# Kernel optimization log

Measured on AMD Instinct MI355X. Metric: run time of the kernel, lower is better.

The kernel has to match this reference:

```python
import jax, jax.numpy as jnp
import numpy as np

DIM = 1024
N = 65536

def _l2norm(x):
    # F.normalize: x / max(||x||_2, eps) along last dim, eps=1e-12
    n = jnp.linalg.norm(x, axis=-1, keepdims=True)
    return x / jnp.maximum(n, 1e-12)

def setup_inputs() -> dict:
    key = jax.random.key(0)
    ks = jax.random.split(key, 10)
    s = 0.02
    return {
        "q_init": jax.random.normal(ks[0], (1, DIM), jnp.float32),
        "k_init": jax.random.normal(ks[1], (N, DIM), jnp.float32),
        "Wq": jax.random.normal(ks[2], (DIM, DIM // 2), jnp.float32) * s,
        "bq": jnp.zeros((DIM // 2,), jnp.float32),
        "Wk": jax.random.normal(ks[3], (DIM, DIM // 2), jnp.float32) * s,
        "bk": jnp.zeros((DIM // 2,), jnp.float32),
        "Wv": jax.random.normal(ks[4], (DIM, DIM), jnp.float32) * s,
        "bv": jnp.zeros((DIM,), jnp.float32),
        "Wm": jax.random.normal(ks[5], (DIM, DIM), jnp.float32) * s,
        "bm": jnp.zeros((DIM,), jnp.float32),
        "gamma": jnp.ones((1,), jnp.float32),
    }

def reference(q_init, k_init, Wq, bq, Wk, bk, Wv, bv, Wm, bm, gamma):
    q = _l2norm(q_init) @ Wq + bq              # [1, dim/2]
    kn = _l2norm(k_init)                        # [N, dim]
    k = kn @ Wk + bk                            # [N, dim/2]
    v = kn @ Wv + bv                            # [N, dim]
    scores = q @ k.T                            # [1, N]
    # global mean/std rescale (torch.std is unbiased, ddof=1)
    scores = (scores - scores.mean()) / (jnp.std(scores, ddof=1) + 1e-8)
    attn = jax.nn.softmax(jnp.clip(scores, -10.0, 10.0), axis=-1)
    # dropout is identity in eval mode
    out = (attn @ v) @ Wm + bm                  # [1, dim]
    g = jax.nn.sigmoid(gamma)                   # [1]
    return g * q_init + (1.0 - g) * out
```

## Files before the change

### kernel.cpp

```cpp
#include <hip/hip_runtime.h>
#include <math.h>

#define DIM   1024
#define HALF  512
#define NROWS 65536
#define SBLK  4096
#define WBLK  1024
#define WF1   32

#define OFF_QN     0
#define OFF_QACC   (OFF_QN + DIM)
#define OFF_PVEC   (OFF_QACC + HALF)
#define OFF_SCAL   (OFF_PVEC + DIM)
#define OFF_PSTAT  (OFF_SCAL + 8)
#define OFF_S      (OFF_PSTAT + 2*SBLK)
#define OFF_INVN   (OFF_S + NROWS)
#define OFF_COEFF  (OFF_INVN + NROWS)
#define OFF_ESUM   (OFF_COEFF + NROWS)
#define OFF_PW     (OFF_ESUM + 256)
#define OFF_P2     (OFF_PW + WBLK*DIM)
#define OFF_WACC   (OFF_P2 + WF1*DIM)
#define OFF_OVACC  (OFF_WACC + DIM)
#define OFF_OUTACC (OFF_OVACC + DIM)
#define OFF_END    (OFF_OUTACC + DIM)

__global__ void k_qnorm(const float* __restrict__ q_init, float* __restrict__ qn) {
    __shared__ float red[1024];
    int t = threadIdx.x;
    float v = q_init[t];
    red[t] = v * v;
    __syncthreads();
    for (int s = 512; s > 0; s >>= 1) {
        if (t < s) red[t] += red[t + s];
        __syncthreads();
    }
    float inv = 1.0f / fmaxf(sqrtf(red[0]), 1e-12f);
    qn[t] = v * inv;
}

__global__ void k_matvec_col(const float* __restrict__ M,
                             const float* __restrict__ coeff,
                             const float* __restrict__ cbias,
                             float* __restrict__ out,
                             int nrows, int ncols4) {
    __shared__ float4 red[256];
    int t = threadIdx.x, c4 = blockIdx.x;
    const float4* M4 = (const float4*)M;
    float4 acc = make_float4(0.f, 0.f, 0.f, 0.f);
    for (int r = t; r < nrows; r += 256) {
        float c = coeff[r];
        if (cbias) c += cbias[r];
        float4 m = M4[(size_t)r * ncols4 + c4];
        acc.x += c * m.x; acc.y += c * m.y; acc.z += c * m.z; acc.w += c * m.w;
    }
    red[t] = acc;
    __syncthreads();
    for (int s = 128; s > 0; s >>= 1) {
        if (t < s) {
            red[t].x += red[t + s].x; red[t].y += red[t + s].y;
            red[t].z += red[t + s].z; red[t].w += red[t + s].w;
        }
        __syncthreads();
    }
    if (t == 0) ((float4*)out)[c4] = red[0];
}

__global__ void k_pvec(const float* __restrict__ Wk,
                       const float* __restrict__ qacc,
                       const float* __restrict__ bq,
                       float* __restrict__ pvec) {
    __shared__ float q[HALF];
    int t = threadIdx.x;
    for (int j = t; j < HALF; j += 256) q[j] = qacc[j] + bq[j];
    __syncthreads();
    int wave = t >> 6, lane = t & 63;
    int d = blockIdx.x * 4 + wave;
    const float* row = Wk + (size_t)d * HALF;
    float acc = 0.f;
    #pragma unroll
    for (int j0 = 0; j0 < HALF; j0 += 64) acc += row[j0 + lane] * q[j0 + lane];
    #pragma unroll
    for (int o = 32; o > 0; o >>= 1) acc += __shfl_down(acc, o);
    if (lane == 0) pvec[d] = acc;
}

__global__ void k_scores(const float* __restrict__ K,
                         const float* __restrict__ pvec,
                         float* __restrict__ svals,
                         float* __restrict__ invn,
                         float2* __restrict__ pstat) {
    __shared__ float4 p4s[256];
    __shared__ float wsum[4], wssq[4];
    int t = threadIdx.x;
    p4s[t] = ((const float4*)pvec)[t];
    __syncthreads();
    int wave = t >> 6, lane = t & 63;
    int row0 = blockIdx.x * 16 + wave * 4;
    const float4* k4 = (const float4*)K + (size_t)row0 * 256;
    float d0 = 0, d1 = 0, d2 = 0, d3 = 0;
    float q0 = 0, q1 = 0, q2 = 0, q3 = 0;
    #pragma unroll
    for (int i = 0; i < 4; ++i) {
        int idx = lane + i * 64;
        float4 p = p4s[idx];
        float4 a = k4[idx];
        float4 b = k4[256 + idx];
        float4 c = k4[512 + idx];
        float4 e = k4[768 + idx];
        d0 += a.x * p.x + a.y * p.y + a.z * p.z + a.w * p.w;
        q0 += a.x * a.x + a.y * a.y + a.z * a.z + a.w * a.w;
        d1 += b.x * p.x + b.y * p.y + b.z * p.z + b.w * p.w;
        q1 += b.x * b.x + b.y * b.y + b.z * b.z + b.w * b.w;
        d2 += c.x * p.x + c.y * p.y + c.z * p.z + c.w * p.w;
        q2 += c.x * c.x + c.y * c.y + c.z * c.z + c.w * c.w;
        d3 += e.x * p.x + e.y * p.y + e.z * p.z + e.w * p.w;
        q3 += e.x * e.x + e.y * e.y + e.z * e.z + e.w * e.w;
    }
    #pragma unroll
    for (int o = 32; o > 0; o >>= 1) {
        d0 += __shfl_down(d0, o); q0 += __shfl_down(q0, o);
        d1 += __shfl_down(d1, o); q1 += __shfl_down(q1, o);
        d2 += __shfl_down(d2, o); q2 += __shfl_down(q2, o);
        d3 += __shfl_down(d3, o); q3 += __shfl_down(q3, o);
    }
    if (lane == 0) {
        float i0 = 1.0f / fmaxf(sqrtf(q0), 1e-12f);
        float i1 = 1.0f / fmaxf(sqrtf(q1), 1e-12f);
        float i2 = 1.0f / fmaxf(sqrtf(q2), 1e-12f);
        float i3 = 1.0f / fmaxf(sqrtf(q3), 1e-12f);
        float s0 = d0 * i0, s1 = d1 * i1, s2 = d2 * i2, s3 = d3 * i3;
        float4 sv = make_float4(s0, s1, s2, s3);
        float4 iv = make_float4(i0, i1, i2, i3);
        *(float4*)(svals + row0) = sv;
        *(float4*)(invn + row0) = iv;
        wsum[wave] = s0 + s1 + s2 + s3;
        wssq[wave] = s0 * s0 + s1 * s1 + s2 * s2 + s3 * s3;
    }
    __syncthreads();
    if (t == 0)
        pstat[blockIdx.x] = make_float2(wsum[0] + wsum[1] + wsum[2] + wsum[3],
                                        wssq[0] + wssq[1] + wssq[2] + wssq[3]);
}

__global__ void k_redstats(const float2* __restrict__ pstat, float* __restrict__ scal) {
    __shared__ float rs[1024], rq[1024];
    int t = threadIdx.x;
    float s = 0.f, q = 0.f;
    for (int i = t; i < SBLK; i += 1024) {
        float2 p = pstat[i];
        s += p.x; q += p.y;
    }
    rs[t] = s; rq[t] = q;
    __syncthreads();
    for (int k = 512; k > 0; k >>= 1) {
        if (t < k) { rs[t] += rs[t + k]; rq[t] += rq[t + k]; }
        __syncthreads();
    }
    if (t == 0) {
        float mean = rs[0] / (float)NROWS;
        float var  = (rq[0] - (float)NROWS * mean * mean) / (float)(NROWS - 1);
        scal[0] = mean;
        scal[1] = 1.0f / (sqrtf(fmaxf(var, 0.0f)) + 1e-8f);
    }
}

__global__ void k_coeff(const float* __restrict__ svals,
                        const float* __restrict__ invn,
                        const float* __restrict__ scal,
                        float* __restrict__ coeff,
                        float* __restrict__ esum) {
    __shared__ float red[256];
    int t = threadIdx.x;
    int i = blockIdx.x * 256 + t;
    float mean = scal[0], rstd = scal[1];
    float z = (svals[i] - mean) * rstd;
    z = fminf(fmaxf(z, -10.0f), 10.0f);
    float e = expf(z);
    coeff[i] = e * invn[i];
    red[t] = e;
    __syncthreads();
    for (int s = 128; s > 0; s >>= 1) {
        if (t < s) red[t] += red[t + s];
        __syncthreads();
    }
    if (t == 0) esum[blockIdx.x] = red[0];
}

__global__ void k_wsum(const float* __restrict__ K,
                       const float* __restrict__ coeff,
                       float* __restrict__ pw) {
    int t = threadIdx.x;
    int r0 = blockIdx.x * 64;
    const float4* M4 = (const float4*)K + (size_t)r0 * 256 + t;
    const float* cf = coeff + r0;
    float4 acc = make_float4(0.f, 0.f, 0.f, 0.f);
    #pragma unroll 16
    for (int r = 0; r < 64; ++r) {
        float c = cf[r];
        float4 m = M4[(size_t)r * 256];
        acc.x += c * m.x; acc.y += c * m.y; acc.z += c * m.z; acc.w += c * m.w;
    }
    ((float4*)pw)[(size_t)blockIdx.x * 256 + t] = acc;
}

__global__ void k_wfold(const float* __restrict__ pw, float* __restrict__ p2) {
    int t = threadIdx.x, b = blockIdx.x;
    const float4* pw4 = (const float4*)pw;
    float4 acc = make_float4(0.f, 0.f, 0.f, 0.f);
    #pragma unroll
    for (int p = 0; p < WBLK / WF1; ++p) {
        float4 m = pw4[(size_t)(b * (WBLK / WF1) + p) * 256 + t];
        acc.x += m.x; acc.y += m.y; acc.z += m.z; acc.w += m.w;
    }
    ((float4*)p2)[b * 256 + t] = acc;
}

__global__ void k_wreduce(const float* __restrict__ p2,
                          const float* __restrict__ esum,
                          float* __restrict__ wacc) {
    __shared__ float red[256];
    int t = threadIdx.x;
    if (t < 256) red[t] = esum[t];
    __syncthreads();
    for (int s = 128; s > 0; s >>= 1) {
        if (t < s) red[t] += red[t + s];
        __syncthreads();
    }
    float inv = 1.0f / red[0];
    float acc = 0.f;
    #pragma unroll
    for (int b = 0; b < WF1; ++b) acc += p2[b * DIM + t];
    wacc[t] = acc * inv;
}

__global__ void k_final(const float* __restrict__ q_init,
                        const float* __restrict__ outacc,
                        const float* __restrict__ bm,
                        const float* __restrict__ gamma,
                        float* __restrict__ out) {
    int t = threadIdx.x;
    float g = 1.0f / (1.0f + expf(-gamma[0]));
    out[t] = g * q_init[t] + (1.0f - g) * (outacc[t] + bm[t]);
}

extern "C" void kernel_launch(void* const* d_in, const int* in_sizes, int n_in,
                              void* d_out, int out_size, void* d_ws, size_t ws_size,
                              hipStream_t stream) {
    const float* q_init = (const float*)d_in[0];
    const float* k_init = (const float*)d_in[1];
    const float* Wq     = (const float*)d_in[2];
    const float* bq     = (const float*)d_in[3];
    const float* Wk     = (const float*)d_in[4];
    const float* Wv     = (const float*)d_in[6];
    const float* bv     = (const float*)d_in[7];
    const float* Wm     = (const float*)d_in[8];
    const float* bm     = (const float*)d_in[9];
    const float* gamma  = (const float*)d_in[10];
    float* out = (float*)d_out;
    float* ws  = (float*)d_ws;

    float*  qn     = ws + OFF_QN;
    float*  qacc   = ws + OFF_QACC;
    float*  pvec   = ws + OFF_PVEC;
    float*  scal   = ws + OFF_SCAL;
    float2* pstat  = (float2*)(ws + OFF_PSTAT);
    float*  svals  = ws + OFF_S;
    float*  invn   = ws + OFF_INVN;
    float*  coeff  = ws + OFF_COEFF;
    float*  esum   = ws + OFF_ESUM;
    float*  pw     = ws + OFF_PW;
    float*  p2     = ws + OFF_P2;
    float*  wacc   = ws + OFF_WACC;
    float*  ovacc  = ws + OFF_OVACC;
    float*  outacc = ws + OFF_OUTACC;

    k_qnorm<<<1, 1024, 0, stream>>>(q_init, qn);
    k_matvec_col<<<HALF / 4, 256, 0, stream>>>(Wq, qn, nullptr, qacc, DIM, HALF / 4);
    k_pvec<<<DIM / 4, 256, 0, stream>>>(Wk, qacc, bq, pvec);
    k_scores<<<SBLK, 256, 0, stream>>>(k_init, pvec, svals, invn, pstat);
    k_redstats<<<1, 1024, 0, stream>>>(pstat, scal);
    k_coeff<<<NROWS / 256, 256, 0, stream>>>(svals, invn, scal, coeff, esum);
    k_wsum<<<WBLK, 256, 0, stream>>>(k_init, coeff, pw);
    k_wfold<<<WF1, 256, 0, stream>>>(pw, p2);
    k_wreduce<<<1, 1024, 0, stream>>>(p2, esum, wacc);
    k_matvec_col<<<DIM / 4, 256, 0, stream>>>(Wv, wacc, nullptr, ovacc, DIM, DIM / 4);
    k_matvec_col<<<DIM / 4, 256, 0, stream>>>(Wm, ovacc, bv, outacc, DIM, DIM / 4);
    k_final<<<1, 1024, 0, stream>>>(q_init, outacc, bm, gamma, out);
}
```

Baseline: 464.1 us.

## Fuse whole pipeline into one cooperative kernel with grid syncs

```diff
diff --git a/kernel.cpp b/kernel.cpp
--- a/kernel.cpp
+++ b/kernel.cpp
@@ -1,12 +1,295 @@
 #include <hip/hip_runtime.h>
+#include <hip/hip_cooperative_groups.h>
 #include <math.h>
+
+namespace cg = cooperative_groups;
 
 #define DIM   1024
 #define HALF  512
 #define NROWS 65536
-#define SBLK  4096
-#define WBLK  1024
-#define WF1   32
+
+#define GRID  1024
+#define RPB   (NROWS / GRID)
+
+#define FOFF_QACC  0
+#define FOFF_PVEC  (FOFF_QACC + HALF)
+#define FOFF_PSTAT (FOFF_PVEC + DIM)
+#define FOFF_ESUM  (FOFF_PSTAT + 2*GRID)
+#define FOFF_WACC  (FOFF_ESUM + GRID)
+#define FOFF_OV    (FOFF_WACC + DIM)
+#define FOFF_PW    (FOFF_OV + DIM)
+
+__global__ __launch_bounds__(256, 4)
+void k_fused(const float* __restrict__ q_init,
+             const float* __restrict__ K,
+             const float* __restrict__ Wq,
+             const float* __restrict__ bq,
+             const float* __restrict__ Wk,
+             const float* __restrict__ Wv,
+             const float* __restrict__ bv,
+             const float* __restrict__ Wm,
+             const float* __restrict__ bm,
+             const float* __restrict__ gamma,
+             float* ws,
+             float* out)
+{
+    cg::grid_group grid = cg::this_grid();
+    const int t = threadIdx.x;
+    const int b = blockIdx.x;
+    const int wave = t >> 6, lane = t & 63;
+
+    float*  qacc  = ws + FOFF_QACC;
+    float*  pvec  = ws + FOFF_PVEC;
+    float2* pstat = (float2*)(ws + FOFF_PSTAT);
+    float*  esum  = ws + FOFF_ESUM;
+    float*  wacc  = ws + FOFF_WACC;
+    float*  ov    = ws + FOFF_OV;
+    float*  pw    = ws + FOFF_PW;
+
+    __shared__ float4 sh4[256];
+    __shared__ float  shA[256];
+    __shared__ float  shB[256];
+    __shared__ float  shq[HALF];
+    __shared__ float  cf[RPB];
+    __shared__ float  ssv[RPB];
+    __shared__ float  siv[RPB];
+    __shared__ float  bc[2];
+
+    if (b < HALF / 4) {
+        float v0 = q_init[t], v1 = q_init[t + 256],
+              v2 = q_init[t + 512], v3 = q_init[t + 768];
+        shA[t] = v0 * v0 + v1 * v1 + v2 * v2 + v3 * v3;
+        __syncthreads();
+        for (int s = 128; s > 0; s >>= 1) {
+            if (t < s) shA[t] += shA[t + s];
+            __syncthreads();
+        }
+        float qinv = 1.0f / fmaxf(sqrtf(shA[0]), 1e-12f);
+        const float4* W4 = (const float4*)Wq;
+        float vv0 = v0 * qinv, vv1 = v1 * qinv, vv2 = v2 * qinv, vv3 = v3 * qinv;
+        float4 acc = make_float4(0.f, 0.f, 0.f, 0.f);
+        float4 m0 = W4[(size_t)t * (HALF / 4) + b];
+        float4 m1 = W4[(size_t)(t + 256) * (HALF / 4) + b];
+        float4 m2 = W4[(size_t)(t + 512) * (HALF / 4) + b];
+        float4 m3 = W4[(size_t)(t + 768) * (HALF / 4) + b];
+        acc.x = vv0 * m0.x + vv1 * m1.x + vv2 * m2.x + vv3 * m3.x;
+        acc.y = vv0 * m0.y + vv1 * m1.y + vv2 * m2.y + vv3 * m3.y;
+        acc.z = vv0 * m0.z + vv1 * m1.z + vv2 * m2.z + vv3 * m3.z;
+        acc.w = vv0 * m0.w + vv1 * m1.w + vv2 * m2.w + vv3 * m3.w;
+        sh4[t] = acc;
+        __syncthreads();
+        for (int s = 128; s > 0; s >>= 1) {
+            if (t < s) {
+                sh4[t].x += sh4[t + s].x; sh4[t].y += sh4[t + s].y;
+                sh4[t].z += sh4[t + s].z; sh4[t].w += sh4[t + s].w;
+            }
+            __syncthreads();
+        }
+        if (t == 0) ((float4*)qacc)[b] = sh4[0];
+    }
+    grid.sync();
+
+    if (b < DIM / 4) {
+        for (int j = t; j < HALF; j += 256) shq[j] = qacc[j] + bq[j];
+        __syncthreads();
+        int d = b * 4 + wave;
+        const float* row = Wk + (size_t)d * HALF;
+        float acc = 0.f;
+        #pragma unroll
+        for (int j0 = 0; j0 < HALF; j0 += 64) acc += row[j0 + lane] * shq[j0 + lane];
+        #pragma unroll
+        for (int o = 32; o > 0; o >>= 1) acc += __shfl_down(acc, o);
+        if (lane == 0) pvec[d] = acc;
+    }
+    grid.sync();
+
+    {
+        sh4[t] = ((const float4*)pvec)[t];
+        __syncthreads();
+        float bsum = 0.f, bssq = 0.f;
+        #pragma unroll 1
+        for (int it = 0; it < 4; ++it) {
+            const int row0 = b * 64 + it * 16 + wave * 4;
+            const float4* k4 = (const float4*)K + (size_t)row0 * 256;
+            float d0 = 0.f, d1 = 0.f, d2 = 0.f, d3 = 0.f;
+            float q0 = 0.f, q1 = 0.f, q2 = 0.f, q3 = 0.f;
+            #pragma unroll
+            for (int i = 0; i < 4; ++i) {
+                const int idx = lane + i * 64;
+                float4 p = sh4[idx];
+                float4 a = k4[idx];
+                float4 bb = k4[256 + idx];
+                float4 c = k4[512 + idx];
+                float4 e = k4[768 + idx];
+                d0 += a.x * p.x + a.y * p.y + a.z * p.z + a.w * p.w;
+                q0 += a.x * a.x + a.y * a.y + a.z * a.z + a.w * a.w;
+                d1 += bb.x * p.x + bb.y * p.y + bb.z * p.z + bb.w * p.w;
+                q1 += bb.x * bb.x + bb.y * bb.y + bb.z * bb.z + bb.w * bb.w;
+                d2 += c.x * p.x + c.y * p.y + c.z * p.z + c.w * p.w;
+                q2 += c.x * c.x + c.y * c.y + c.z * c.z + c.w * c.w;
+                d3 += e.x * p.x + e.y * p.y + e.z * p.z + e.w * p.w;
+                q3 += e.x * e.x + e.y * e.y + e.z * e.z + e.w * e.w;
+            }
+            #pragma unroll
+            for (int o = 32; o > 0; o >>= 1) {
+                d0 += __shfl_down(d0, o); q0 += __shfl_down(q0, o);
+                d1 += __shfl_down(d1, o); q1 += __shfl_down(q1, o);
+                d2 += __shfl_down(d2, o); q2 += __shfl_down(q2, o);
+                d3 += __shfl_down(d3, o); q3 += __shfl_down(q3, o);
+            }
+            if (lane == 0) {
+                float i0 = 1.0f / fmaxf(sqrtf(q0), 1e-12f);
+                float i1 = 1.0f / fmaxf(sqrtf(q1), 1e-12f);
+                float i2 = 1.0f / fmaxf(sqrtf(q2), 1e-12f);
+                float i3 = 1.0f / fmaxf(sqrtf(q3), 1e-12f);
+                float s0 = d0 * i0, s1 = d1 * i1, s2 = d2 * i2, s3 = d3 * i3;
+                const int o64 = it * 16 + wave * 4;
+                ssv[o64] = s0; ssv[o64 + 1] = s1; ssv[o64 + 2] = s2; ssv[o64 + 3] = s3;
+                siv[o64] = i0; siv[o64 + 1] = i1; siv[o64 + 2] = i2; siv[o64 + 3] = i3;
+                bsum += s0 + s1 + s2 + s3;
+                bssq += s0 * s0 + s1 * s1 + s2 * s2 + s3 * s3;
+            }
+        }
+        if (lane == 0) { shA[wave] = bsum; shB[wave] = bssq; }
+        __syncthreads();
+        if (t == 0)
+            pstat[b] = make_float2(shA[0] + shA[1] + shA[2] + shA[3],
+                                   shB[0] + shB[1] + shB[2] + shB[3]);
+    }
+    grid.sync();
+
+    {
+        float s = 0.f, q = 0.f;
+        #pragma unroll
+        for (int i = 0; i < 4; ++i) {
+            float2 p = pstat[t + i * 256];
+            s += p.x; q += p.y;
+        }
+        shA[t] = s; shB[t] = q;
+        __syncthreads();
+        for (int k = 128; k > 0; k >>= 1) {
+            if (t < k) { shA[t] += shA[t + k]; shB[t] += shB[t + k]; }
+            __syncthreads();
+        }
+        if (t == 0) {
+            float mean = shA[0] / (float)NROWS;
+            float var  = (shB[0] - (float)NROWS * mean * mean) / (float)(NROWS - 1);
+            bc[0] = mean;
+            bc[1] = 1.0f / (sqrtf(fmaxf(var, 0.0f)) + 1e-8f);
+        }
+        __syncthreads();
+        float mean = bc[0], rstd = bc[1];
+        if (t < RPB) {
+            float z = (ssv[t] - mean) * rstd;
+            z = fminf(fmaxf(z, -10.0f), 10.0f);
+            float e = expf(z);
+            cf[t] = e * siv[t];
+            float es = e;
+            #pragma unroll
+            for (int o = 32; o > 0; o >>= 1) es += __shfl_down(es, o);
+            if (t == 0) esum[b] = es;
+        }
+        __syncthreads();
+        const float4* M4 = (const float4*)K + (size_t)(b * 64) * 256 + t;
+        float4 acc = make_float4(0.f, 0.f, 0.f, 0.f);
+        #pragma unroll 16
+        for (int r = 0; r < RPB; ++r) {
+            float c = cf[r];
+            float4 m = M4[(size_t)r * 256];
+            acc.x += c * m.x; acc.y += c * m.y; acc.z += c * m.z; acc.w += c * m.w;
+        }
+        ((float4*)pw)[(size_t)b * 256 + t] = acc;
+    }
+    grid.sync();
+
+    if (b < 256) {
+        float es = esum[t] + esum[t + 256] + esum[t + 512] + esum[t + 768];
+        shA[t] = es;
+        __syncthreads();
+        for (int s = 128; s > 0; s >>= 1) {
+            if (t < s) shA[t] += shA[t + s];
+            __syncthreads();
+        }
+        float inv = 1.0f / shA[0];
+        const float4* pw4 = (const float4*)pw;
+        float4 acc = make_float4(0.f, 0.f, 0.f, 0.f);
+        #pragma unroll
+        for (int j = 0; j < 4; ++j) {
+            float4 m = pw4[(size_t)(t + j * 256) * 256 + b];
+            acc.x += m.x; acc.y += m.y; acc.z += m.z; acc.w += m.w;
+        }
+        sh4[t] = acc;
+        __syncthreads();
+        for (int s = 128; s > 0; s >>= 1) {
+            if (t < s) {
+                sh4[t].x += sh4[t + s].x; sh4[t].y += sh4[t + s].y;
+                sh4[t].z += sh4[t + s].z; sh4[t].w += sh4[t + s].w;
+            }
+            __syncthreads();
+        }
+        if (t == 0) {
+            float4 w = sh4[0];
+            ((float4*)wacc)[b] = make_float4(w.x * inv, w.y * inv, w.z * inv, w.w * inv);
+        }
+    }
+    grid.sync();
+
+    if (b < 256) {
+        const float4* W4 = (const float4*)Wv;
+        float4 acc = make_float4(0.f, 0.f, 0.f, 0.f);
+        for (int r = t; r < DIM; r += 256) {
+            float c = wacc[r];
+            float4 m = W4[(size_t)r * 256 + b];
+            acc.x += c * m.x; acc.y += c * m.y; acc.z += c * m.z; acc.w += c * m.w;
+        }
+        sh4[t] = acc;
+        __syncthreads();
+        for (int s = 128; s > 0; s >>= 1) {
+            if (t < s) {
+                sh4[t].x += sh4[t + s].x; sh4[t].y += sh4[t + s].y;
+                sh4[t].z += sh4[t + s].z; sh4[t].w += sh4[t + s].w;
+            }
+            __syncthreads();
+        }
+        if (t == 0) ((float4*)ov)[b] = sh4[0];
+    }
+    grid.sync();
+
+    if (b < 256) {
+        const float4* W4 = (const float4*)Wm;
+        float4 acc = make_float4(0.f, 0.f, 0.f, 0.f);
+        for (int r = t; r < DIM; r += 256) {
+            float c = ov[r] + bv[r];
+            float4 m = W4[(size_t)r * 256 + b];
+            acc.x += c * m.x; acc.y += c * m.y; acc.z += c * m.z; acc.w += c * m.w;
+        }
+        sh4[t] = acc;
+        __syncthreads();
+        for (int s = 128; s > 0; s >>= 1) {
+            if (t < s) {
+                sh4[t].x += sh4[t + s].x; sh4[t].y += sh4[t + s].y;
+                sh4[t].z += sh4[t + s].z; sh4[t].w += sh4[t + s].w;
+            }
+            __syncthreads();
+        }
+        if (t == 0) {
+            float g = 1.0f / (1.0f + expf(-gamma[0]));
+            float4 o  = sh4[0];
+            float4 qi = ((const float4*)q_init)[b];
+            float4 bb = ((const float4*)bm)[b];
+            float4 res;
+            res.x = g * qi.x + (1.0f - g) * (o.x + bb.x);
+            res.y = g * qi.y + (1.0f - g) * (o.y + bb.y);
+            res.z = g * qi.z + (1.0f - g) * (o.z + bb.z);
+            res.w = g * qi.w + (1.0f - g) * (o.w + bb.w);
+            ((float4*)out)[b] = res;
+        }
+    }
+}
+
+#define SBLK 4096
+#define WBLK 1024
+#define WF1  32
 
 #define OFF_QN     0
 #define OFF_QACC   (OFF_QN + DIM)
@@ -22,7 +305,6 @@
 #define OFF_WACC   (OFF_P2 + WF1*DIM)
 #define OFF_OVACC  (OFF_WACC + DIM)
 #define OFF_OUTACC (OFF_OVACC + DIM)
-#define OFF_END    (OFF_OUTACC + DIM)
 
 __global__ void k_qnorm(const float* __restrict__ q_init, float* __restrict__ qn) {
     __shared__ float red[1024];
@@ -192,11 +474,11 @@
     int t = threadIdx.x;
     int r0 = blockIdx.x * 64;
     const float4* M4 = (const float4*)K + (size_t)r0 * 256 + t;
-    const float* cf = coeff + r0;
+    const float* cfp = coeff + r0;
     float4 acc = make_float4(0.f, 0.f, 0.f, 0.f);
     #pragma unroll 16
     for (int r = 0; r < 64; ++r) {
-        float c = cf[r];
+        float c = cfp[r];
         float4 m = M4[(size_t)r * 256];
         acc.x += c * m.x; acc.y += c * m.y; acc.z += c * m.z; acc.w += c * m.w;
     }
@@ -259,6 +541,13 @@
     float* out = (float*)d_out;
     float* ws  = (float*)d_ws;
 
+    void* args[] = { (void*)&q_init, (void*)&k_init, (void*)&Wq, (void*)&bq,
+                     (void*)&Wk, (void*)&Wv, (void*)&bv, (void*)&Wm,
+                     (void*)&bm, (void*)&gamma, (void*)&ws, (void*)&out };
+    hipError_t err = hipLaunchCooperativeKernel(k_fused, dim3(GRID), dim3(256),
+                                                args, 0, stream);
+    if (err == hipSuccess) return;
+
     float*  qn     = ws + OFF_QN;
     float*  qacc   = ws + OFF_QACC;
     float*  pvec   = ws + OFF_PVEC;
```

Result: slower. 1.130 ms (+143.4%).

## Fuse small pipeline stages to cut kernel launches from twelve to eight

Applied to the files above, without the earlier changes.

```diff
diff --git a/kernel.cpp b/kernel.cpp
--- a/kernel.cpp
+++ b/kernel.cpp
@@ -6,63 +6,55 @@
 #define NROWS 65536
 #define SBLK  4096
 #define WBLK  1024
-#define WF1   32
-
-#define OFF_QN     0
-#define OFF_QACC   (OFF_QN + DIM)
+
+#define OFF_QACC   0
 #define OFF_PVEC   (OFF_QACC + HALF)
-#define OFF_SCAL   (OFF_PVEC + DIM)
-#define OFF_PSTAT  (OFF_SCAL + 8)
+#define OFF_PSTAT  (OFF_PVEC + DIM)
 #define OFF_S      (OFF_PSTAT + 2*SBLK)
 #define OFF_INVN   (OFF_S + NROWS)
 #define OFF_COEFF  (OFF_INVN + NROWS)
 #define OFF_ESUM   (OFF_COEFF + NROWS)
 #define OFF_PW     (OFF_ESUM + 256)
-#define OFF_P2     (OFF_PW + WBLK*DIM)
-#define OFF_WACC   (OFF_P2 + WF1*DIM)
+#define OFF_WACC   (OFF_PW + WBLK*DIM)
 #define OFF_OVACC  (OFF_WACC + DIM)
-#define OFF_OUTACC (OFF_OVACC + DIM)
-#define OFF_END    (OFF_OUTACC + DIM)
-
-__global__ void k_qnorm(const float* __restrict__ q_init, float* __restrict__ qn) {
-    __shared__ float red[1024];
-    int t = threadIdx.x;
-    float v = q_init[t];
-    red[t] = v * v;
-    __syncthreads();
-    for (int s = 512; s > 0; s >>= 1) {
-        if (t < s) red[t] += red[t + s];
-        __syncthreads();
-    }
-    float inv = 1.0f / fmaxf(sqrtf(red[0]), 1e-12f);
-    qn[t] = v * inv;
-}
-
-__global__ void k_matvec_col(const float* __restrict__ M,
-                             const float* __restrict__ coeff,
-                             const float* __restrict__ cbias,
-                             float* __restrict__ out,
-                             int nrows, int ncols4) {
-    __shared__ float4 red[256];
-    int t = threadIdx.x, c4 = blockIdx.x;
-    const float4* M4 = (const float4*)M;
-    float4 acc = make_float4(0.f, 0.f, 0.f, 0.f);
-    for (int r = t; r < nrows; r += 256) {
-        float c = coeff[r];
-        if (cbias) c += cbias[r];
-        float4 m = M4[(size_t)r * ncols4 + c4];
-        acc.x += c * m.x; acc.y += c * m.y; acc.z += c * m.z; acc.w += c * m.w;
-    }
-    red[t] = acc;
+#define OFF_END    (OFF_OVACC + DIM)
+
+__global__ void k_q(const float* __restrict__ q_init,
+                    const float* __restrict__ Wq,
+                    float* __restrict__ qacc) {
+    __shared__ float  shA[256];
+    __shared__ float4 sh4[256];
+    int t = threadIdx.x, b = blockIdx.x;
+    float v0 = q_init[t], v1 = q_init[t + 256],
+          v2 = q_init[t + 512], v3 = q_init[t + 768];
+    shA[t] = v0 * v0 + v1 * v1 + v2 * v2 + v3 * v3;
+    __syncthreads();
+    for (int s = 128; s > 0; s >>= 1) {
+        if (t < s) shA[t] += shA[t + s];
+        __syncthreads();
+    }
+    float qinv = 1.0f / fmaxf(sqrtf(shA[0]), 1e-12f);
+    const float4* W4 = (const float4*)Wq;
+    float vv0 = v0 * qinv, vv1 = v1 * qinv, vv2 = v2 * qinv, vv3 = v3 * qinv;
+    float4 m0 = W4[(size_t)t * (HALF / 4) + b];
+    float4 m1 = W4[(size_t)(t + 256) * (HALF / 4) + b];
+    float4 m2 = W4[(size_t)(t + 512) * (HALF / 4) + b];
+    float4 m3 = W4[(size_t)(t + 768) * (HALF / 4) + b];
+    float4 acc;
+    acc.x = vv0 * m0.x + vv1 * m1.x + vv2 * m2.x + vv3 * m3.x;
+    acc.y = vv0 * m0.y + vv1 * m1.y + vv2 * m2.y + vv3 * m3.y;
+    acc.z = vv0 * m0.z + vv1 * m1.z + vv2 * m2.z + vv3 * m3.z;
+    acc.w = vv0 * m0.w + vv1 * m1.w + vv2 * m2.w + vv3 * m3.w;
+    sh4[t] = acc;
     __syncthreads();
     for (int s = 128; s > 0; s >>= 1) {
         if (t < s) {
-            red[t].x += red[t + s].x; red[t].y += red[t + s].y;
-            red[t].z += red[t + s].z; red[t].w += red[t + s].w;
+            sh4[t].x += sh4[t + s].x; sh4[t].y += sh4[t + s].y;
+            sh4[t].z += sh4[t + s].z; sh4[t].w += sh4[t + s].w;
         }
         __syncthreads();
     }
-    if (t == 0) ((float4*)out)[c4] = red[0];
+    if (t == 0) ((float4*)qacc)[b] = sh4[0];
 }
 
 __global__ void k_pvec(const float* __restrict__ Wk,
@@ -142,48 +134,40 @@
                                         wssq[0] + wssq[1] + wssq[2] + wssq[3]);
 }
 
-__global__ void k_redstats(const float2* __restrict__ pstat, float* __restrict__ scal) {
-    __shared__ float rs[1024], rq[1024];
-    int t = threadIdx.x;
+__global__ void k_coeff2(const float* __restrict__ svals,
+                         const float* __restrict__ invn,
+                         const float2* __restrict__ pstat,
+                         float* __restrict__ coeff,
+                         float* __restrict__ esum) {
+    __shared__ float rs[256], rq[256];
+    int t = threadIdx.x, b = blockIdx.x;
     float s = 0.f, q = 0.f;
-    for (int i = t; i < SBLK; i += 1024) {
+    for (int i = t; i < SBLK; i += 256) {
         float2 p = pstat[i];
         s += p.x; q += p.y;
     }
     rs[t] = s; rq[t] = q;
     __syncthreads();
-    for (int k = 512; k > 0; k >>= 1) {
+    for (int k = 128; k > 0; k >>= 1) {
         if (t < k) { rs[t] += rs[t + k]; rq[t] += rq[t + k]; }
         __syncthreads();
     }
-    if (t == 0) {
-        float mean = rs[0] / (float)NROWS;
-        float var  = (rq[0] - (float)NROWS * mean * mean) / (float)(NROWS - 1);
-        scal[0] = mean;
-        scal[1] = 1.0f / (sqrtf(fmaxf(var, 0.0f)) + 1e-8f);
-    }
-}
-
-__global__ void k_coeff(const float* __restrict__ svals,
-                        const float* __restrict__ invn,
-                        const float* __restrict__ scal,
-                        float* __restrict__ coeff,
-                        float* __restrict__ esum) {
-    __shared__ float red[256];
-    int t = threadIdx.x;
-    int i = blockIdx.x * 256 + t;
-    float mean = scal[0], rstd = scal[1];
+    float mean = rs[0] / (float)NROWS;
+    float var  = (rq[0] - (float)NROWS * mean * mean) / (float)(NROWS - 1);
+    float rstd = 1.0f / (sqrtf(fmaxf(var, 0.0f)) + 1e-8f);
+    int i = b * 256 + t;
     float z = (svals[i] - mean) * rstd;
     z = fminf(fmaxf(z, -10.0f), 10.0f);
     float e = expf(z);
     coeff[i] = e * invn[i];
-    red[t] = e;
-    __syncthreads();
-    for (int s = 128; s > 0; s >>= 1) {
-        if (t < s) red[t] += red[t + s];
-        __syncthreads();
-    }
-    if (t == 0) esum[blockIdx.x] = red[0];
+    __syncthreads();
+    rs[t] = e;
+    __syncthreads();
+    for (int k = 128; k > 0; k >>= 1) {
+        if (t < k) rs[t] += rs[t + k];
+        __syncthreads();
+    }
+    if (t == 0) esum[b] = rs[0];
 }
 
 __global__ void k_wsum(const float* __restrict__ K,
@@ -203,44 +187,105 @@
     ((float4*)pw)[(size_t)blockIdx.x * 256 + t] = acc;
 }
 
-__global__ void k_wfold(const float* __restrict__ pw, float* __restrict__ p2) {
+__global__ void k_wred(const float* __restrict__ pw,
+                       const float* __restrict__ esum,
+                       float* __restrict__ wacc) {
+    __shared__ float  rs[256];
+    __shared__ float4 sh4[256];
     int t = threadIdx.x, b = blockIdx.x;
+    rs[t] = esum[t];
+    __syncthreads();
+    for (int k = 128; k > 0; k >>= 1) {
+        if (t < k) rs[t] += rs[t + k];
+        __syncthreads();
+    }
+    float inv = 1.0f / rs[0];
     const float4* pw4 = (const float4*)pw;
+    int c4 = b * 64 + (t & 63);
+    int qr = t >> 6;
     float4 acc = make_float4(0.f, 0.f, 0.f, 0.f);
-    #pragma unroll
-    for (int p = 0; p < WBLK / WF1; ++p) {
-        float4 m = pw4[(size_t)(b * (WBLK / WF1) + p) * 256 + t];
+    #pragma unroll 8
+    for (int p = qr * 256; p < qr * 256 + 256; ++p) {
+        float4 m = pw4[(size_t)p * 256 + c4];
         acc.x += m.x; acc.y += m.y; acc.z += m.z; acc.w += m.w;
     }
-    ((float4*)p2)[b * 256 + t] = acc;
-}
-
-__global__ void k_wreduce(const float* __restrict__ p2,
-                          const float* __restrict__ esum,
-                          float* __restrict__ wacc) {
-    __shared__ float red[256];
-    int t = threadIdx.x;
-    if (t < 256) red[t] = esum[t];
+    sh4[t] = acc;
+    __syncthreads();
+    if (t < 64) {
+        float4 a = sh4[t], b4 = sh4[t + 64], c = sh4[t + 128], d = sh4[t + 192];
+        float4 w;
+        w.x = (a.x + b4.x + c.x + d.x) * inv;
+        w.y = (a.y + b4.y + c.y + d.y) * inv;
+        w.z = (a.z + b4.z + c.z + d.z) * inv;
+        w.w = (a.w + b4.w + c.w + d.w) * inv;
+        ((float4*)wacc)[b * 64 + t] = w;
+    }
+}
+
+__global__ void k_matvec_col(const float* __restrict__ M,
+                             const float* __restrict__ coeff,
+                             const float* __restrict__ cbias,
+                             float* __restrict__ out,
+                             int nrows, int ncols4) {
+    __shared__ float4 red[256];
+    int t = threadIdx.x, c4 = blockIdx.x;
+    const float4* M4 = (const float4*)M;
+    float4 acc = make_float4(0.f, 0.f, 0.f, 0.f);
+    for (int r = t; r < nrows; r += 256) {
+        float c = coeff[r];
+        if (cbias) c += cbias[r];
+        float4 m = M4[(size_t)r * ncols4 + c4];
+        acc.x += c * m.x; acc.y += c * m.y; acc.z += c * m.z; acc.w += c * m.w;
+    }
+    red[t] = acc;
     __syncthreads();
     for (int s = 128; s > 0; s >>= 1) {
-        if (t < s) red[t] += red[t + s];
-        __syncthreads();
-    }
-    float inv = 1.0f / red[0];
-    float acc = 0.f;
-    #pragma unroll
-    for (int b = 0; b < WF1; ++b) acc += p2[b * DIM + t];
-    wacc[t] = acc * inv;
-}
-
-__global__ void k_final(const float* __restrict__ q_init,
-                        const float* __restrict__ outacc,
-                        const float* __restrict__ bm,
-                        const float* __restrict__ gamma,
-                        float* __restrict__ out) {
-    int t = threadIdx.x;
-    float g = 1.0f / (1.0f + expf(-gamma[0]));
-    out[t] = g * q_init[t] + (1.0f - g) * (outacc[t] + bm[t]);
+        if (t < s) {
+            red[t].x += red[t + s].x; red[t].y += red[t + s].y;
+            red[t].z += red[t + s].z; red[t].w += red[t + s].w;
+        }
+        __syncthreads();
+    }
+    if (t == 0) ((float4*)out)[c4] = red[0];
+}
+
+__global__ void k_mv_final(const float* __restrict__ Wm,
+                           const float* __restrict__ ovacc,
+                           const float* __restrict__ bv,
+                           const float* __restrict__ q_init,
+                           const float* __restrict__ bm,
+                           const float* __restrict__ gamma,
+                           float* __restrict__ out) {
+    __shared__ float4 sh4[256];
+    int t = threadIdx.x, b = blockIdx.x;
+    const float4* W4 = (const float4*)Wm;
+    float4 acc = make_float4(0.f, 0.f, 0.f, 0.f);
+    for (int r = t; r < DIM; r += 256) {
+        float c = ovacc[r] + bv[r];
+        float4 m = W4[(size_t)r * 256 + b];
+        acc.x += c * m.x; acc.y += c * m.y; acc.z += c * m.z; acc.w += c * m.w;
+    }
+    sh4[t] = acc;
+    __syncthreads();
+    for (int s = 128; s > 0; s >>= 1) {
+        if (t < s) {
+            sh4[t].x += sh4[t + s].x; sh4[t].y += sh4[t + s].y;
+            sh4[t].z += sh4[t + s].z; sh4[t].w += sh4[t + s].w;
+        }
+        __syncthreads();
+    }
+    if (t == 0) {
+        float g = 1.0f / (1.0f + expf(-gamma[0]));
+        float4 o  = sh4[0];
+        float4 qi = ((const float4*)q_init)[b];
+        float4 bb = ((const float4*)bm)[b];
+        float4 res;
+        res.x = g * qi.x + (1.0f - g) * (o.x + bb.x);
+        res.y = g * qi.y + (1.0f - g) * (o.y + bb.y);
+        res.z = g * qi.z + (1.0f - g) * (o.z + bb.z);
+        res.w = g * qi.w + (1.0f - g) * (o.w + bb.w);
+        ((float4*)out)[b] = res;
+    }
 }
 
 extern "C" void kernel_launch(void* const* d_in, const int* in_sizes, int n_in,
@@ -259,31 +304,23 @@
     float* out = (float*)d_out;
     float* ws  = (float*)d_ws;
 
-    float*  qn     = ws + OFF_QN;
     float*  qacc   = ws + OFF_QACC;
     float*  pvec   = ws + OFF_PVEC;
-    float*  scal   = ws + OFF_SCAL;
     float2* pstat  = (float2*)(ws + OFF_PSTAT);
     float*  svals  = ws + OFF_S;
     float*  invn   = ws + OFF_INVN;
     float*  coeff  = ws + OFF_COEFF;
     float*  esum   = ws + OFF_ESUM;
     float*  pw     = ws + OFF_PW;
-    float*  p2     = ws + OFF_P2;
     float*  wacc   = ws + OFF_WACC;
     float*  ovacc  = ws + OFF_OVACC;
-    float*  outacc = ws + OFF_OUTACC;
-
-    k_qnorm<<<1, 1024, 0, stream>>>(q_init, qn);
-    k_matvec_col<<<HALF / 4, 256, 0, stream>>>(Wq, qn, nullptr, qacc, DIM, HALF / 4);
+
+    k_q<<<HALF / 4, 256, 0, stream>>>(q_init, Wq, qacc);
     k_pvec<<<DIM / 4, 256, 0, stream>>>(Wk, qacc, bq, pvec);
     k_scores<<<SBLK, 256, 0, stream>>>(k_init, pvec, svals, invn, pstat);
-    k_redstats<<<1, 1024, 0, stream>>>(pstat, scal);
-    k_coeff<<<NROWS / 256, 256, 0, stream>>>(svals, invn, scal, coeff, esum);
+    k_coeff2<<<NROWS / 256, 256, 0, stream>>>(svals, invn, pstat, coeff, esum);
     k_wsum<<<WBLK, 256, 0, stream>>>(k_init, coeff, pw);
-    k_wfold<<<WF1, 256, 0, stream>>>(pw, p2);
-    k_wreduce<<<1, 1024, 0, stream>>>(p2, esum, wacc);
+    k_wred<<<4, 256, 0, stream>>>(pw, esum, wacc);
     k_matvec_col<<<DIM / 4, 256, 0, stream>>>(Wv, wacc, nullptr, ovacc, DIM, DIM / 4);
-    k_matvec_col<<<DIM / 4, 256, 0, stream>>>(Wm, ovacc, bv, outacc, DIM, DIM / 4);
-    k_final<<<1, 1024, 0, stream>>>(q_init, outacc, bm, gamma, out);
-}
+    k_mv_final<<<DIM / 4, 256, 0, stream>>>(Wm, ovacc, bv, q_init, bm, gamma, out);
+}
```

Measured after the change: 477.1 us. 2.8% more time.
